# Kernel tuning notes

Measured on AMD Instinct MI355X. Metric: run time of the kernel, lower is better.

Reference implementation:

```python
import jax, jax.numpy as jnp
import numpy as np

N_NODES, LATENT_DIM = 16, 8
BOX = 10.0                      # periodic box size (minimum-image convention)
BATCH = 32768
N_POLY, N_SELECT = 1000, 512
SOFT = 1e-3                     # softening constant
POWERS = (2, 3, 4, 5, 6, 8, 10, 12, 14)

# static index sets (constants, match torch.triu_indices offset=1 ordering)
IU, JU = np.triu_indices(N_NODES, k=1)      # node pairs, P = 120
II, JJ = np.triu_indices(LATENT_DIM, k=1)   # intra-latent dim pairs, 28


def setup_inputs() -> dict:
    key = jax.random.key(0)
    k1, k2, k3, k4 = jax.random.split(key, 4)
    D = N_NODES * LATENT_DIM
    return {
        "z_flat": jax.random.normal(k1, (BATCH, D), jnp.float32),
        "z_mean": jax.random.normal(k2, (D,), jnp.float32),
        "z_std": jnp.ones((D,), jnp.float32),
        "x_poly_mean": jax.random.normal(k3, (N_POLY,), jnp.float32),
        "x_poly_std": jnp.ones((N_POLY,), jnp.float32),
        "feature_mask": jax.random.randint(k4, (N_SELECT,), 0, N_POLY, jnp.int32),
    }


def reference(z_flat, z_mean, z_std, x_poly_mean, x_poly_std, feature_mask):
    z = jnp.clip(z_flat, -1e6, 1e6)
    B = z.shape[0]
    zn = (z - z_mean) / z_std                       # normalized raw latents [B, 128]
    nodes = z.reshape(B, N_NODES, LATENT_DIM)

    # --- pairwise distance features on first 2 latent dims, minimum image ---
    diff = nodes[:, IU, :2] - nodes[:, JU, :2]      # [B, P, 2]
    diff = diff - BOX * jnp.round(diff / BOX)
    d = jnp.sqrt(jnp.sum(diff * diff, axis=2)) + 1e-6   # [B, P]
    e = jnp.exp(-d)
    dist = [d, 1.0 / (d + SOFT)]
    dist += [1.0 / (d ** n + SOFT) for n in POWERS]
    dist += [e, e / (d + SOFT), jnp.log(d + SOFT)]

    X = jnp.clip(jnp.concatenate([zn] + dist, axis=1), -1e6, 1e6)   # [B, 1808]

    # --- physics-informed expansion ---
    Xn = zn.reshape(B, N_NODES, LATENT_DIM)
    p_sq = jnp.sum(Xn[:, :, LATENT_DIM // 2:] ** 2, axis=2)         # [B, 16]
    intra = (Xn[:, :, II] * Xn[:, :, JJ]).reshape(B, -1)            # [B, 16*28]
    inter = (Xn[:, IU, :] * Xn[:, JU, :]).reshape(B, -1)            # [B, 120*8]
    Xe = jnp.concatenate([
        X, zn ** 2, jnp.sin(zn), jnp.cos(zn),
        jnp.log(jnp.abs(zn) + 1e-3), jnp.exp(jnp.clip(zn, -10, 2)),
        p_sq, intra, inter,
    ], axis=1)                                                       # [B, 3872]

    # variance-based top-1000 selection (unbiased variance, as torch.var)
    if Xe.shape[1] > N_POLY:
        var = jnp.var(Xe, axis=0, ddof=1)
        _, top = jax.lax.top_k(var, N_POLY)
        Xe = Xe[:, top]

    Xe = jnp.clip(jnp.nan_to_num(Xe, nan=0.0, posinf=1e9, neginf=-1e9), -1e12, 1e12)

    # masked selection + normalization
    sel = Xe[:, feature_mask]
    return (sel - x_poly_mean[feature_mask]) / x_poly_std[feature_mask]
```

## Files before the change

### kernel.cpp

```cpp
#include <hip/hip_runtime.h>
#include <cstdint>
#include <cstddef>

#define NFEAT 3872
#define NPAIR 120
#define NB    32768
#define ZD    128
#define NPOLY 1000
#define NSEL  512
#define SOFT  1e-3f

#define STHREADS 512
#define NZSLOT   1856
#define ZCHUNK   4
#define SB       64
#define RO       8
#define VCHUNK   32
#define RSLICE   32
#define RGSZ     121
#define MAXT     1984


__device__ __forceinline__ float frcp(float x) {
  float r = __builtin_amdgcn_rcpf(x);
  float e = fmaf(-x, r, 1.0f);
  return fmaf(r, e, r);
}

#define FSIN(x) __sinf(x)
#define FCOS(x) __cosf(x)
#define FLOG(x) __logf(x)
#define FEXP(x) __expf(x)

__device__ __forceinline__ void init_tables_par(int tid, unsigned char* IUs, unsigned char* JUs,
                                                unsigned char* IIs, unsigned char* JJs) {
  if (tid < NPAIR) {
    int i = 0, rem = tid;
    while (rem >= 15 - i) { rem -= 15 - i; ++i; }
    IUs[tid] = (unsigned char)i; JUs[tid] = (unsigned char)(i + 1 + rem);
  }
  if (tid < 28) {
    int i = 0, rem = tid;
    while (rem >= 7 - i) { rem -= 7 - i; ++i; }
    IIs[tid] = (unsigned char)i; JJs[tid] = (unsigned char)(i + 1 + rem);
  }
}

__device__ __forceinline__ int pack_plan(int f, const unsigned char* IUs, const unsigned char* JUs,
                                         const unsigned char* IIs, const unsigned char* JJs) {
  int op = 31, a0 = 0, a1 = 0;
  if (f < 128) { op = 0; a0 = f; }
  else if (f < 1808) { int t = f - 128; int b = t / 120; int p = t - b * 120; op = 1 + b; a0 = p; }
  else if (f < 1936) { op = 15; a0 = f - 1808; }
  else if (f < 2064) { op = 16; a0 = f - 1936; }
  else if (f < 2192) { op = 17; a0 = f - 2064; }
  else if (f < 2320) { op = 18; a0 = f - 2192; }
  else if (f < 2448) { op = 19; a0 = f - 2320; }
  else if (f < 2464) { op = 20; a0 = (f - 2448) * 8; }
  else if (f < 2912) { int t = f - 2464; int n = t / 28; int qq = t - n * 28;
                       op = 21; a0 = n * 8 + IIs[qq]; a1 = n * 8 + JJs[qq]; }
  else if (f < NFEAT) { int t = f - 2912; int p = t >> 3; int kk = t & 7;
                        op = 21; a0 = IUs[p] * 8 + kk; a1 = JUs[p] * 8 + kk; }
  return op | (a0 << 5) | (a1 << 12);
}

__device__ __forceinline__ int decode_zslot(int s, const unsigned char* IUs, const unsigned char* JUs,
                                            const unsigned char* IIs, const unsigned char* JJs) {
  int op = 0, a0 = 0, a1 = 0, fid = 4095;
  if (s < 128) { op = 1; a0 = s; fid = s; }
  else if (s < 256) { op = 2; a0 = s - 128; fid = 1936 + (s - 128); }
  else if (s < 384) { op = 3; a0 = s - 256; fid = 2192 + (s - 256); }
  else if (s < 448) {
    int q = s - 384;
    op = 4;
    a0 = (q < 16) ? q * 8 : 0;
    if (q < 16) fid = 2448 + q;
  } else if (s < 896) {
    int t = s - 448;
    int n = t / 28, qq = t - n * 28;
    op = 5; a0 = n * 8 + IIs[qq]; a1 = n * 8 + JJs[qq]; fid = 2464 + t;
  } else if (s < NZSLOT) {
    int t = s - 896;
    int p = t >> 3, kk = t & 7;
    op = 5; a0 = IUs[p] * 8 + kk; a1 = JUs[p] * 8 + kk; fid = 2912 + t;
  }
  return op | (a0 << 3) | (a1 << 10) | (fid << 17);
}

__global__ __launch_bounds__(STHREADS) void stats_kernel(const float* __restrict__ z,
                                                         const float* __restrict__ zmean,
                                                         const float* __restrict__ zstd,
                                                         float* __restrict__ psum,
                                                         float* __restrict__ psumsq,
                                                         int rows_per_block) {
  __shared__ __align__(16) union {
    struct { float zm[ZD]; float rz[ZD]; float zn[SB * ZD]; } zns;
    struct { float zc[SB * 32]; float red[4][2 * NPAIR]; } ds;
  } sh;
  __shared__ unsigned char IUs[NPAIR], JUs[NPAIR], IIs[28], JJs[28];
  int tid = threadIdx.x;
  init_tables_par(tid, IUs, JUs, IIs, JJs);
  int bx = blockIdx.x;
  int b = bx >> 1;
  int row0 = b * rows_per_block;
  int row1 = min(row0 + rows_per_block, NB);

  if ((bx & 1) == 0) {
    if (tid < ZD) { sh.zns.zm[tid] = zmean[tid]; sh.zns.rz[tid] = frcp(zstd[tid]); }
    __syncthreads();

    int plan[ZCHUNK];
#pragma unroll
    for (int k = 0; k < ZCHUNK; ++k)
      plan[k] = decode_zslot(tid + k * STHREADS, IUs, JUs, IIs, JJs);

    float s[ZCHUNK], q[ZCHUNK], s2 = 0.0f, q2 = 0.0f;
#pragma unroll
    for (int k = 0; k < ZCHUNK; ++k) { s[k] = 0.0f; q[k] = 0.0f; }

#define ROWLOOP _Pragma("unroll 8") for (int rr = 0; rr < SB; ++rr)
#define ACC  { sk += v; qk = fmaf(v, v, qk); }
#define ACC2 { sk2 += v2; qk2 = fmaf(v2, v2, qk2); }

    for (int r0 = row0; r0 < row1; r0 += SB) {
      const float4* z4 = (const float4*)(z + (size_t)r0 * ZD);
#pragma unroll
      for (int u = 0; u < SB * ZD / 4 / STHREADS; ++u) {
        int t = u * STHREADS + tid;
        float4 v = z4[t];
        int c4 = t & 31;
        v.x = fminf(fmaxf(v.x, -1e6f), 1e6f);
        v.y = fminf(fmaxf(v.y, -1e6f), 1e6f);
        v.z = fminf(fmaxf(v.z, -1e6f), 1e6f);
        v.w = fminf(fmaxf(v.w, -1e6f), 1e6f);
        float4 m4 = ((const float4*)sh.zns.zm)[c4];
        float4 r4 = ((const float4*)sh.zns.rz)[c4];
        float4 o;
        o.x = (v.x - m4.x) * r4.x;
        o.y = (v.y - m4.y) * r4.y;
        o.z = (v.z - m4.z) * r4.z;
        o.w = (v.w - m4.w) * r4.w;
        ((float4*)sh.zns.zn)[t] = o;
      }
      __syncthreads();
      const float* znS = sh.zns.zn;
      {
        int pk = plan[0];
        int a0 = (pk >> 3) & 127, a1 = (pk >> 10) & 127;
        int wop = __builtin_amdgcn_readfirstlane(pk & 7);
        float sk = 0.0f, qk = 0.0f, sk2 = 0.0f, qk2 = 0.0f;
        switch (wop) {
          case 1: ROWLOOP { float v = znS[rr * ZD + a0];
                            float v2 = v * v; ACC ACC2 } break;
          case 2: ROWLOOP { float x = znS[rr * ZD + a0];
                            float v, v2; __sincosf(x, &v, &v2); ACC ACC2 } break;
          case 3: ROWLOOP { float x = znS[rr * ZD + a0];
                            float v = FLOG(fabsf(x) + 0.001f);
                            float xc = fminf(fmaxf(x, -10.0f), 2.0f);
                            float v2 = FEXP(xc); ACC ACC2 } break;
          case 4: ROWLOOP { const float* zr = znS + rr * ZD + a0;
                            float x4 = zr[4]; float x5 = zr[5]; float x6 = zr[6]; float x7 = zr[7];
                            float v = x4 * x4 + x5 * x5 + x6 * x6 + x7 * x7; ACC } break;
          case 5: ROWLOOP { const float* zr = znS + rr * ZD; float v = zr[a0] * zr[a1]; ACC } break;
          default: break;
        }
        s[0] += sk; q[0] += qk;
        if (wop >= 1 && wop <= 3) { s2 += sk2; q2 += qk2; }
      }
#pragma unroll
      for (int k = 1; k < ZCHUNK; ++k) {
        int pk = plan[k];
        int a0 = (pk >> 3) & 127, a1 = (pk >> 10) & 127;
        int act = __builtin_amdgcn_readfirstlane((int)(((pk >> 17) & 4095) != 4095));
        if (act) {
          float sk = 0.0f, qk = 0.0f;
          ROWLOOP { const float* zr = znS + rr * ZD; float v = zr[a0] * zr[a1]; ACC }
          s[k] += sk; q[k] += qk;
        }
      }
      __syncthreads();
    }
#undef ROWLOOP
#undef ACC
#undef ACC2

#pragma unroll
    for (int k = 0; k < ZCHUNK; ++k) {
      int fid = (plan[k] >> 17) & 4095;
      int opk = plan[k] & 7;
      if (fid != 4095) {
        psum[(size_t)b * NFEAT + fid] = s[k];
        psumsq[(size_t)b * NFEAT + fid] = q[k];
        if (k == 0 && opk >= 1 && opk <= 3) {
          int fid2 = fid + ((opk == 1) ? 1808 : 128);
          psum[(size_t)b * NFEAT + fid2] = s2;
          psumsq[(size_t)b * NFEAT + fid2] = q2;
        }
      }
    }
  } else {
    __syncthreads();
    int p  = tid & 127;
    int rg = tid >> 7;
    int ni = (p < NPAIR) ? IUs[p] : 0;
    int nj = (p < NPAIR) ? JUs[p] : 0;

    float sF[14], qF[14];
#pragma unroll
    for (int bb = 0; bb < 14; ++bb) { sF[bb] = 0.0f; qF[bb] = 0.0f; }

    for (int r0 = row0; r0 < row1; r0 += SB) {
#pragma unroll
      for (int u = 0; u < SB * 32 / STHREADS; ++u) {
        int t = u * STHREADS + tid;
        int rr = t >> 5, c = t & 31;
        int col = ((c >> 1) << 3) + (c & 1);
        float v = z[(size_t)(r0 + rr) * ZD + col];
        sh.ds.zc[t] = fminf(fmaxf(v, -1e6f), 1e6f);
      }
      __syncthreads();
      if (p < NPAIR) {
        for (int rr = rg; rr < SB; rr += 4) {
          const float* zc = sh.ds.zc + rr * 32;
          float dx = zc[ni * 2 + 0] - zc[nj * 2 + 0];
          float dy = zc[ni * 2 + 1] - zc[nj * 2 + 1];
          dx = fmaf(-10.0f, rintf(dx * 0.1f), dx);
          dy = fmaf(-10.0f, rintf(dy * 0.1f), dy);
          float d = sqrtf(dx * dx + dy * dy) + 1e-6f;
          float e = FEXP(-d);
          float d2 = d * d,   d3 = d2 * d,  d4 = d2 * d2, d5 = d4 * d, d6 = d4 * d2;
          float d8 = d4 * d4, d10 = d8 * d2, d12 = d8 * d4, d14 = d12 * d2;
          float r1 = frcp(d + SOFT);
          float v[14];
          v[0]  = d;
          v[1]  = r1;
          v[2]  = frcp(d2 + SOFT);
          v[3]  = frcp(d3 + SOFT);
          v[4]  = frcp(d4 + SOFT);
          v[5]  = frcp(d5 + SOFT);
          v[6]  = frcp(d6 + SOFT);
          v[7]  = frcp(d8 + SOFT);
          v[8]  = frcp(d10 + SOFT);
          v[9]  = frcp(d12 + SOFT);
          v[10] = frcp(d14 + SOFT);
          v[11] = e;
          v[12] = e * r1;
          v[13] = FLOG(d + SOFT);
#pragma unroll
          for (int bb = 0; bb < 14; ++bb) {
            sF[bb] += v[bb];
            qF[bb] = fmaf(v[bb], v[bb], qF[bb]);
          }
        }
      }
      __syncthreads();
    }

    for (int bb = 0; bb < 14; ++bb) {
      if (p < NPAIR) {
        sh.ds.red[rg][p] = sF[bb];
        sh.ds.red[rg][NPAIR + p] = qF[bb];
      }
      __syncthreads();
      if (tid < 2 * NPAIR) {
        float t2 = ((sh.ds.red[0][tid] + sh.ds.red[1][tid]) + sh.ds.red[2][tid]) + sh.ds.red[3][tid];
        if (tid < NPAIR) psum[(size_t)b * NFEAT + 128 + bb * 120 + tid] = t2;
        else             psumsq[(size_t)b * NFEAT + 128 + bb * 120 + (tid - NPAIR)] = t2;
      }
      __syncthreads();
    }
  }
}

__global__ __launch_bounds__(256) void var1_kernel(const float* __restrict__ psum,
                                                   const float* __restrict__ psumsq,
                                                   double* __restrict__ psum2,
                                                   double* __restrict__ psumsq2,
                                                   int* __restrict__ rankA,
                                                   int slices) {
  int f = blockIdx.x * 256 + threadIdx.x;
  if (f >= NFEAT) return;
  if (blockIdx.y == 0) rankA[f] = 0;
  int b0 = blockIdx.y * slices;
  double s = 0.0, q = 0.0;
  for (int b = b0; b < b0 + slices; ++b) {
    s += (double)psum[(size_t)b * NFEAT + f];
    q += (double)psumsq[(size_t)b * NFEAT + f];
  }
  psum2[(size_t)blockIdx.y * NFEAT + f] = s;
  psumsq2[(size_t)blockIdx.y * NFEAT + f] = q;
}

__global__ __launch_bounds__(256) void var2rank1_kernel(const double* __restrict__ psum2,
                                                        const double* __restrict__ psumsq2,
                                                        int chunks,
                                                        int* __restrict__ rankA) {
  __shared__ double gvS[RGSZ];
  int tid = threadIdx.x;
  int g0 = blockIdx.y * RGSZ;
  const double N = (double)NB;
  if (tid < RGSZ) {
    double s = 0.0, q = 0.0;
    for (int b = 0; b < chunks; ++b) {
      s += psum2[(size_t)b * NFEAT + g0 + tid];
      q += psumsq2[(size_t)b * NFEAT + g0 + tid];
    }
    gvS[tid] = (q - s * s / N) / (N - 1.0);
  }
  __syncthreads();
  int f = blockIdx.x * 256 + tid;
  if (f >= NFEAT) return;
  double s = 0.0, q = 0.0;
  for (int b = 0; b < chunks; ++b) {
    s += psum2[(size_t)b * NFEAT + f];
    q += psumsq2[(size_t)b * NFEAT + f];
  }
  double vf = (q - s * s / N) / (N - 1.0);
  int cnt = 0;
#pragma unroll 11
  for (int k = 0; k < RGSZ; ++k) {
    double vg = gvS[k];
    int g = g0 + k;
    cnt += (int)((vg > vf) || (vg == vf && g < f));
  }
  atomicAdd(&rankA[f], cnt);
}

__global__ __launch_bounds__(1024) void rank2map_kernel(const int* __restrict__ rankA,
                                                        const int* __restrict__ mask,
                                                        const float* __restrict__ pmean,
                                                        const float* __restrict__ pstd,
                                                        int* __restrict__ taskW,
                                                        float* __restrict__ taskA,
                                                        float* __restrict__ taskB,
                                                        int* __restrict__ ntaskW) {
  __shared__ int topcolS[NPOLY];
  __shared__ int taskS[MAXT];
  __shared__ int cntS[32], pstartS[32];
  __shared__ int wcntS[8][32], wbaseS[8][32];
  __shared__ unsigned char IUs[NPAIR], JUs[NPAIR], IIs[28], JJs[28];
  int tid = threadIdx.x;
  init_tables_par(tid, IUs, JUs, IIs, JJs);
  for (int i = tid; i < MAXT; i += 1024) { taskS[i] = 31; taskA[i] = 0.0f; taskB[i] = 0.0f; }
  for (int f = tid; f < NFEAT; f += 1024) {
    int r = rankA[f];
    if (r < NPOLY) topcolS[r] = f;
  }
  __syncthreads();
  int pk = 31, op = 31;
  float aN = 0.0f, bN = 0.0f;
  int wave = tid >> 6, lane = tid & 63;
  unsigned long long mymask = 0;
  if (tid < NSEL) {
    int m = mask[tid];
    int c = topcolS[m];
    aN = frcp(pstd[m]);
    bN = -pmean[m] * aN;
    pk = pack_plan(c, IUs, JUs, IIs, JJs);
    op = pk & 31;
    for (int o = 0; o < 32; ++o) {
      unsigned long long bm = __ballot(op == o);
      if (lane == 0) wcntS[wave][o] = __popcll(bm);
      if (op == o) mymask = bm;
    }
  }
  __syncthreads();
  if (tid < 32) {
    int c = 0;
    for (int w2 = 0; w2 < 8; ++w2) { wbaseS[w2][tid] = c; c += wcntS[w2][tid]; }
    cntS[tid] = c;
  }
  __syncthreads();
  if (tid == 0) {
    int pcum = 0;
    for (int o = 0; o < 32; ++o) {
      pstartS[o] = pcum;
      pcum += (cntS[o] + 63) / 64 * 64;
    }
    ntaskW[0] = pcum;
  }
  __syncthreads();
  if (tid < NSEL) {
    int slot = pstartS[op] + wbaseS[wave][op]
             + (int)__popcll(mymask & ((1ull << lane) - 1ull));
    taskS[slot] = pk | (tid << 19);
    taskA[slot] = aN;
    taskB[slot] = bN;
  }
  __syncthreads();
  for (int i = tid; i < MAXT; i += 1024) taskW[i] = taskS[i];
}

__global__ __launch_bounds__(256) void out_kernel(const float* __restrict__ z,
                                                  const float* __restrict__ zmean,
                                                  const float* __restrict__ zstd,
                                                  const int* __restrict__ taskW,
                                                  const float* __restrict__ taskA,
                                                  const float* __restrict__ taskB,
                                                  const int* __restrict__ ntaskW,
                                                  float* __restrict__ out,
                                                  int rows_per_block) {
  __shared__ __align__(16) float zmS[ZD];
  __shared__ __align__(16) float rzS[ZD];
  __shared__ __align__(16) float znS[RO * ZD];
  __shared__ float zcS[RO * 32], dS[RO * NPAIR];
  __shared__ __align__(16) float rowS[RO * NSEL];
  __shared__ unsigned char IUs[NPAIR], JUs[NPAIR], IIs[28], JJs[28];
  int tid = threadIdx.x;
  int row0 = blockIdx.x * rows_per_block;
  int row1 = min(row0 + rows_per_block, NB);
  const float4* z4 = (const float4*)(z + (size_t)row0 * ZD);
  float4 cur = z4[tid];
  init_tables_par(tid, IUs, JUs, IIs, JJs);
  if (tid < ZD) { zmS[tid] = zmean[tid]; rzS[tid] = frcp(zstd[tid]); }
  int ntask = ntaskW[0];
  __syncthreads();

  int nbat = (row1 - row0) / RO;
  for (int t2 = 0; t2 < nbat; ++t2) {
    int r0 = row0 + t2 * RO;
    {
      float4 v = cur;
      int rr = tid >> 5, c4 = tid & 31;
      v.x = fminf(fmaxf(v.x, -1e6f), 1e6f);
      v.y = fminf(fmaxf(v.y, -1e6f), 1e6f);
      v.z = fminf(fmaxf(v.z, -1e6f), 1e6f);
      v.w = fminf(fmaxf(v.w, -1e6f), 1e6f);
      if ((c4 & 1) == 0) {
        int node = c4 >> 1;
        zcS[rr * 32 + node * 2 + 0] = v.x;
        zcS[rr * 32 + node * 2 + 1] = v.y;
      }
      float4 m4 = ((const float4*)zmS)[c4];
      float4 s4 = ((const float4*)rzS)[c4];
      float4 o;
      o.x = (v.x - m4.x) * s4.x;
      o.y = (v.y - m4.y) * s4.y;
      o.z = (v.z - m4.z) * s4.z;
      o.w = (v.w - m4.w) * s4.w;
      ((float4*)znS)[tid] = o;
    }
    if (t2 + 1 < nbat) cur = z4[(size_t)(t2 + 1) * (RO * ZD / 4) + tid];
    __syncthreads();
    for (int t = tid; t < RO * 128; t += 256) {
      int p = t & 127;
      if (p < NPAIR) {
        int rr = t >> 7;
        int i = IUs[p], j = JUs[p];
        float dx = zcS[rr * 32 + i * 2 + 0] - zcS[rr * 32 + j * 2 + 0];
        float dy = zcS[rr * 32 + i * 2 + 1] - zcS[rr * 32 + j * 2 + 1];
        dx = fmaf(-10.0f, rintf(dx * 0.1f), dx);
        dy = fmaf(-10.0f, rintf(dy * 0.1f), dy);
        dS[rr * NPAIR + p] = sqrtf(dx * dx + dy * dy) + 1e-6f;
      }
    }
    __syncthreads();
#define RLV(BODY) { _Pragma("unroll") for (int rr = 0; rr < RO; ++rr) { \
      const float* znR = znS + rr * ZD; const float* dR = dS + rr * NPAIR; \
      (void)znR; (void)dR; float v; BODY; \
      if (valid) rowS[rr * NSEL + dst] = fmaf(v, aA, bA); } } break;
    for (int s2 = tid; s2 < ntask; s2 += 256) {
      int pk = taskW[s2];
      float aA = taskA[s2], bA = taskB[s2];
      int op = pk & 31;
      int a0 = (pk >> 5) & 127, a1 = (pk >> 12) & 127, dst = (pk >> 19) & 511;
      bool valid = (op != 31);
      int wop = __builtin_amdgcn_readfirstlane(op);
      switch (wop) {
        case 0:  RLV({ v = znR[a0]; })
        case 1:  RLV({ v = dR[a0]; })
        case 2:  RLV({ float d = dR[a0]; v = frcp(d + SOFT); })
        case 3:  RLV({ float d = dR[a0]; v = frcp(d * d + SOFT); })
        case 4:  RLV({ float d = dR[a0]; float d2 = d * d; v = frcp(d2 * d + SOFT); })
        case 5:  RLV({ float d = dR[a0]; float d2 = d * d; v = frcp(d2 * d2 + SOFT); })
        case 6:  RLV({ float d = dR[a0]; float d2 = d * d; float d4 = d2 * d2; v = frcp(d4 * d + SOFT); })
        case 7:  RLV({ float d = dR[a0]; float d2 = d * d; float d4 = d2 * d2; v = frcp(d4 * d2 + SOFT); })
        case 8:  RLV({ float d = dR[a0]; float d2 = d * d; float d4 = d2 * d2; v = frcp(d4 * d4 + SOFT); })
        case 9:  RLV({ float d = dR[a0]; float d2 = d * d; float d4 = d2 * d2; float d8 = d4 * d4; v = frcp(d8 * d2 + SOFT); })
        case 10: RLV({ float d = dR[a0]; float d2 = d * d; float d4 = d2 * d2; float d8 = d4 * d4; v = frcp(d8 * d4 + SOFT); })
        case 11: RLV({ float d = dR[a0]; float d2 = d * d; float d4 = d2 * d2; float d8 = d4 * d4; v = frcp(d8 * d4 * d2 + SOFT); })
        case 12: RLV({ v = FEXP(-dR[a0]); })
        case 13: RLV({ float d = dR[a0]; v = FEXP(-d) * frcp(d + SOFT); })
        case 14: RLV({ v = FLOG(dR[a0] + SOFT); })
        case 15: RLV({ float x = znR[a0]; v = x * x; })
        case 16: RLV({ v = FSIN(znR[a0]); })
        case 17: RLV({ v = FCOS(znR[a0]); })
        case 18: RLV({ v = FLOG(fabsf(znR[a0]) + 0.001f); })
        case 19: RLV({ float x = znR[a0]; x = fminf(fmaxf(x, -10.0f), 2.0f); v = FEXP(x); })
        case 20: RLV({ const float* zr = znR + a0;
                       float x4 = zr[4]; float x5 = zr[5]; float x6 = zr[6]; float x7 = zr[7];
                       v = x4 * x4 + x5 * x5 + x6 * x6 + x7 * x7; })
        case 21:
        case 22: RLV({ v = znR[a0] * znR[a1]; })
        default: break;
      }
    }
#undef RLV
    __syncthreads();
    {
      float4* o4 = (float4*)(out + (size_t)r0 * NSEL);
      const float4* r4 = (const float4*)rowS;
      for (int t = tid; t < RO * NSEL / 4; t += 256) o4[t] = r4[t];
    }
    __syncthreads();
  }
}

extern "C" void kernel_launch(void* const* d_in, const int* in_sizes, int n_in,
                              void* d_out, int out_size, void* d_ws, size_t ws_size,
                              hipStream_t stream) {
  const float* z     = (const float*)d_in[0];
  const float* zmean = (const float*)d_in[1];
  const float* zstd  = (const float*)d_in[2];
  const float* pmean = (const float*)d_in[3];
  const float* pstd  = (const float*)d_in[4];
  const int*   mask  = (const int*)d_in[5];
  float* out = (float*)d_out;

  size_t tail = (size_t)VCHUNK * NFEAT * 16 + (size_t)NFEAT * 4
              + MAXT * 12 + 4096;
  int G = 512;
  while (G > 1 && (size_t)G * NFEAT * 8 + tail > ws_size) G >>= 1;
  int chunks = (G < VCHUNK) ? G : VCHUNK;
  int slices = G / chunks;

  char* w = (char*)d_ws;
  float*  psum    = (float*)w;                 w += (size_t)G * NFEAT * 4;
  float*  psumsq  = (float*)w;                 w += (size_t)G * NFEAT * 4;
  double* psum2   = (double*)w;                w += (size_t)VCHUNK * NFEAT * 8;
  double* psumsq2 = (double*)w;                w += (size_t)VCHUNK * NFEAT * 8;
  int*    rankA   = (int*)w;                   w += (size_t)NFEAT * 4;
  int*    taskW   = (int*)w;                   w += MAXT * 4;
  float*  taskA   = (float*)w;                 w += MAXT * 4;
  float*  taskB   = (float*)w;                 w += MAXT * 4;
  int*    ntaskW  = (int*)w;

  int rpb_stats = NB / G;
  stats_kernel<<<dim3(2 * G), dim3(STHREADS), 0, stream>>>(z, zmean, zstd, psum, psumsq,
                                                           rpb_stats);
  var1_kernel<<<dim3((NFEAT + 255) / 256, chunks), dim3(256), 0, stream>>>(psum, psumsq,
                                                                           psum2, psumsq2,
                                                                           rankA, slices);
  var2rank1_kernel<<<dim3((NFEAT + 255) / 256, RSLICE), dim3(256), 0, stream>>>(psum2, psumsq2,
                                                                                chunks, rankA);
  rank2map_kernel<<<dim3(1), dim3(1024), 0, stream>>>(rankA, mask, pmean, pstd,
                                                      taskW, taskA, taskB, ntaskW);
  const int rpb_out = 16;
  out_kernel<<<dim3(NB / rpb_out), dim3(256), 0, stream>>>(z, zmean, zstd, taskW, taskA, taskB,
                                                           ntaskW, out, rpb_out);
}
```

Measured before the change: 87.59 us.

## Merge task opcodes, prefetch next task, double rows per block

Collapses the 22 per-feature opcodes into 12 groups. The nine inverse-power features now share one opcode that builds d^n from bit flags in a1, and the square feature reuses the product opcode. Tasks are padded to 64 per opcode, so fewer opcode buckets means fewer padded idle tasks, and MAXT shrinks to match. It also software-prefetches the next task descriptor, adds an occupancy hint to launch_bounds, and processes 32 rows per block instead of 16, which halves the grid. The merged power path adds selects and extra multiplies on every power feature, and the larger row count per block may reduce parallelism.

Measured after the change: 84.37 us. -3.7%, faster.

```diff
diff --git a/kernel.cpp b/kernel.cpp
--- a/kernel.cpp
+++ b/kernel.cpp
@@ -18,7 +18,7 @@
 #define VCHUNK   32
 #define RSLICE   32
 #define RGSZ     121
-#define MAXT     1984
+#define MAXT     1280
 
 
 __device__ __forceinline__ float frcp(float x) {
@@ -50,17 +50,27 @@
                                          const unsigned char* IIs, const unsigned char* JJs) {
   int op = 31, a0 = 0, a1 = 0;
   if (f < 128) { op = 0; a0 = f; }
-  else if (f < 1808) { int t = f - 128; int b = t / 120; int p = t - b * 120; op = 1 + b; a0 = p; }
-  else if (f < 1936) { op = 15; a0 = f - 1808; }
-  else if (f < 2064) { op = 16; a0 = f - 1936; }
-  else if (f < 2192) { op = 17; a0 = f - 2064; }
-  else if (f < 2320) { op = 18; a0 = f - 2192; }
-  else if (f < 2448) { op = 19; a0 = f - 2320; }
-  else if (f < 2464) { op = 20; a0 = (f - 2448) * 8; }
+  else if (f < 1808) {
+    int t = f - 128; int b = t / 120; int p = t - b * 120; a0 = p;
+    if (b == 0) op = 1;
+    else if (b == 11) op = 3;
+    else if (b == 12) op = 4;
+    else if (b == 13) op = 5;
+    else {
+      const int P[10] = {1, 2, 3, 4, 5, 6, 8, 10, 12, 14};
+      op = 2; a1 = P[b - 1];
+    }
+  }
+  else if (f < 1936) { op = 11; a0 = f - 1808; a1 = a0; }
+  else if (f < 2064) { op = 6; a0 = f - 1936; }
+  else if (f < 2192) { op = 7; a0 = f - 2064; }
+  else if (f < 2320) { op = 8; a0 = f - 2192; }
+  else if (f < 2448) { op = 9; a0 = f - 2320; }
+  else if (f < 2464) { op = 10; a0 = (f - 2448) * 8; }
   else if (f < 2912) { int t = f - 2464; int n = t / 28; int qq = t - n * 28;
-                       op = 21; a0 = n * 8 + IIs[qq]; a1 = n * 8 + JJs[qq]; }
+                       op = 11; a0 = n * 8 + IIs[qq]; a1 = n * 8 + JJs[qq]; }
   else if (f < NFEAT) { int t = f - 2912; int p = t >> 3; int kk = t & 7;
-                        op = 21; a0 = IUs[p] * 8 + kk; a1 = JUs[p] * 8 + kk; }
+                        op = 11; a0 = IUs[p] * 8 + kk; a1 = JUs[p] * 8 + kk; }
   return op | (a0 << 5) | (a1 << 12);
 }
 
@@ -391,15 +401,15 @@
   for (int i = tid; i < MAXT; i += 1024) taskW[i] = taskS[i];
 }
 
-__global__ __launch_bounds__(256) void out_kernel(const float* __restrict__ z,
-                                                  const float* __restrict__ zmean,
-                                                  const float* __restrict__ zstd,
-                                                  const int* __restrict__ taskW,
-                                                  const float* __restrict__ taskA,
-                                                  const float* __restrict__ taskB,
-                                                  const int* __restrict__ ntaskW,
-                                                  float* __restrict__ out,
-                                                  int rows_per_block) {
+__global__ __launch_bounds__(256, 6) void out_kernel(const float* __restrict__ z,
+                                                     const float* __restrict__ zmean,
+                                                     const float* __restrict__ zstd,
+                                                     const int* __restrict__ taskW,
+                                                     const float* __restrict__ taskA,
+                                                     const float* __restrict__ taskB,
+                                                     const int* __restrict__ ntaskW,
+                                                     float* __restrict__ out,
+                                                     int rows_per_block) {
   __shared__ __align__(16) float zmS[ZD];
   __shared__ __align__(16) float rzS[ZD];
   __shared__ __align__(16) float znS[RO * ZD];
@@ -459,40 +469,44 @@
       const float* znR = znS + rr * ZD; const float* dR = dS + rr * NPAIR; \
       (void)znR; (void)dR; float v; BODY; \
       if (valid) rowS[rr * NSEL + dst] = fmaf(v, aA, bA); } } break;
-    for (int s2 = tid; s2 < ntask; s2 += 256) {
-      int pk = taskW[s2];
-      float aA = taskA[s2], bA = taskB[s2];
-      int op = pk & 31;
-      int a0 = (pk >> 5) & 127, a1 = (pk >> 12) & 127, dst = (pk >> 19) & 511;
-      bool valid = (op != 31);
-      int wop = __builtin_amdgcn_readfirstlane(op);
-      switch (wop) {
-        case 0:  RLV({ v = znR[a0]; })
-        case 1:  RLV({ v = dR[a0]; })
-        case 2:  RLV({ float d = dR[a0]; v = frcp(d + SOFT); })
-        case 3:  RLV({ float d = dR[a0]; v = frcp(d * d + SOFT); })
-        case 4:  RLV({ float d = dR[a0]; float d2 = d * d; v = frcp(d2 * d + SOFT); })
-        case 5:  RLV({ float d = dR[a0]; float d2 = d * d; v = frcp(d2 * d2 + SOFT); })
-        case 6:  RLV({ float d = dR[a0]; float d2 = d * d; float d4 = d2 * d2; v = frcp(d4 * d + SOFT); })
-        case 7:  RLV({ float d = dR[a0]; float d2 = d * d; float d4 = d2 * d2; v = frcp(d4 * d2 + SOFT); })
-        case 8:  RLV({ float d = dR[a0]; float d2 = d * d; float d4 = d2 * d2; v = frcp(d4 * d4 + SOFT); })
-        case 9:  RLV({ float d = dR[a0]; float d2 = d * d; float d4 = d2 * d2; float d8 = d4 * d4; v = frcp(d8 * d2 + SOFT); })
-        case 10: RLV({ float d = dR[a0]; float d2 = d * d; float d4 = d2 * d2; float d8 = d4 * d4; v = frcp(d8 * d4 + SOFT); })
-        case 11: RLV({ float d = dR[a0]; float d2 = d * d; float d4 = d2 * d2; float d8 = d4 * d4; v = frcp(d8 * d4 * d2 + SOFT); })
-        case 12: RLV({ v = FEXP(-dR[a0]); })
-        case 13: RLV({ float d = dR[a0]; v = FEXP(-d) * frcp(d + SOFT); })
-        case 14: RLV({ v = FLOG(dR[a0] + SOFT); })
-        case 15: RLV({ float x = znR[a0]; v = x * x; })
-        case 16: RLV({ v = FSIN(znR[a0]); })
-        case 17: RLV({ v = FCOS(znR[a0]); })
-        case 18: RLV({ v = FLOG(fabsf(znR[a0]) + 0.001f); })
-        case 19: RLV({ float x = znR[a0]; x = fminf(fmaxf(x, -10.0f), 2.0f); v = FEXP(x); })
-        case 20: RLV({ const float* zr = znR + a0;
-                       float x4 = zr[4]; float x5 = zr[5]; float x6 = zr[6]; float x7 = zr[7];
-                       v = x4 * x4 + x5 * x5 + x6 * x6 + x7 * x7; })
-        case 21:
-        case 22: RLV({ v = znR[a0] * znR[a1]; })
-        default: break;
+    {
+      int s2 = tid;
+      int pk = 31; float aA = 0.0f, bA = 0.0f;
+      if (s2 < ntask) { pk = taskW[s2]; aA = taskA[s2]; bA = taskB[s2]; }
+      for (; s2 < ntask; s2 += 256) {
+        int s2n = s2 + 256;
+        int pk_n = 31; float aA_n = 0.0f, bA_n = 0.0f;
+        if (s2n < ntask) { pk_n = taskW[s2n]; aA_n = taskA[s2n]; bA_n = taskB[s2n]; }
+        int op = pk & 31;
+        int a0 = (pk >> 5) & 127, a1 = (pk >> 12) & 127, dst = (pk >> 19) & 511;
+        bool valid = (op != 31);
+        int wop = __builtin_amdgcn_readfirstlane(op);
+        switch (wop) {
+          case 0:  RLV({ v = znR[a0]; })
+          case 1:  RLV({ v = dR[a0]; })
+          case 2:  RLV({ float d = dR[a0];
+                         float d2 = d * d;
+                         float d4 = d2 * d2;
+                         float d8 = d4 * d4;
+                         float acc = (a1 & 8) ? d8 : 1.0f;
+                         acc *= (a1 & 4) ? d4 : 1.0f;
+                         acc *= (a1 & 2) ? d2 : 1.0f;
+                         acc *= (a1 & 1) ? d  : 1.0f;
+                         v = frcp(acc + SOFT); })
+          case 3:  RLV({ v = FEXP(-dR[a0]); })
+          case 4:  RLV({ float d = dR[a0]; v = FEXP(-d) * frcp(d + SOFT); })
+          case 5:  RLV({ v = FLOG(dR[a0] + SOFT); })
+          case 6:  RLV({ v = FSIN(znR[a0]); })
+          case 7:  RLV({ v = FCOS(znR[a0]); })
+          case 8:  RLV({ v = FLOG(fabsf(znR[a0]) + 0.001f); })
+          case 9:  RLV({ float x = znR[a0]; x = fminf(fmaxf(x, -10.0f), 2.0f); v = FEXP(x); })
+          case 10: RLV({ const float* zr = znR + a0;
+                         float x4 = zr[4]; float x5 = zr[5]; float x6 = zr[6]; float x7 = zr[7];
+                         v = x4 * x4 + x5 * x5 + x6 * x6 + x7 * x7; })
+          case 11: RLV({ v = znR[a0] * znR[a1]; })
+          default: break;
+        }
+        pk = pk_n; aA = aA_n; bA = bA_n;
       }
     }
 #undef RLV
@@ -545,7 +559,7 @@
                                                                                 chunks, rankA);
   rank2map_kernel<<<dim3(1), dim3(1024), 0, stream>>>(rankA, mask, pmean, pstd,
                                                       taskW, taskA, taskB, ntaskW);
-  const int rpb_out = 16;
+  const int rpb_out = 32;
   out_kernel<<<dim3(NB / rpb_out), dim3(256), 0, stream>>>(z, zmean, zstd, taskW, taskA, taskB,
                                                            ntaskW, out, rpb_out);
 }
```
